# Optimization experiments

Hardware: AMD Instinct MI355X
Metric: run time of the kernel (lower is better)

Reference implementation:

```python
import jax, jax.numpy as jnp
import numpy as np

NSAMPLE = 64  # init kwarg nsample
BN_EPS = 1e-5


def setup_inputs() -> dict:
    key = jax.random.key(0)
    ks = jax.random.split(key, 8)
    B, N = 8, 4096
    C_IN, NC = 6, 3
    NP = 1024
    M = [64, 64, 128]
    C0 = C_IN + NC
    xyz = jax.random.normal(ks[0], (B, 3, N), dtype=jnp.float32)
    points = jax.random.normal(ks[1], (B, C_IN, N), dtype=jnp.float32)
    one_hot_vec = jax.nn.one_hot(jax.random.randint(ks[2], (B,), 0, NC), NC, dtype=jnp.float32)
    idx = jax.random.randint(ks[3], (B, NP), 0, N, dtype=jnp.int64)
    w1 = jax.random.normal(ks[4], (M[0], C0), dtype=jnp.float32) * (1.0 / np.sqrt(C0))
    w2 = jax.random.normal(ks[5], (M[1], M[0]), dtype=jnp.float32) * (1.0 / np.sqrt(M[0]))
    w3 = jax.random.normal(ks[6], (M[2], M[1]), dtype=jnp.float32) * (1.0 / np.sqrt(M[1]))
    g1, b1 = jnp.ones((M[0],), jnp.float32), jnp.zeros((M[0],), jnp.float32)
    g2, b2 = jnp.ones((M[1],), jnp.float32), jnp.zeros((M[1],), jnp.float32)
    g3, b3 = jnp.ones((M[2],), jnp.float32), jnp.zeros((M[2],), jnp.float32)
    return {"xyz": xyz, "points": points, "one_hot_vec": one_hot_vec, "idx": idx,
            "w1": w1, "g1": g1, "b1": b1, "w2": w2, "g2": g2, "b2": b2,
            "w3": w3, "g3": g3, "b3": b3}


def _conv_bn_relu(x, w, gamma, beta):
    # x: (B, C, NP, NS); w: (O, C) -- 1x1 conv, no bias; BN with batch stats (train mode)
    y = jnp.einsum('oc,bcpn->bopn', w, x)
    mu = jnp.mean(y, axis=(0, 2, 3), keepdims=True)
    var = jnp.var(y, axis=(0, 2, 3), keepdims=True)
    y = (y - mu) * jax.lax.rsqrt(var + BN_EPS)
    y = y * gamma[None, :, None, None] + beta[None, :, None, None]
    return jax.nn.relu(y)


def reference(xyz, points, one_hot_vec, idx, w1, g1, b1, w2, g2, b2, w3, g3, b3):
    B, _, N = xyz.shape
    NP = idx.shape[1]
    NS = NSAMPLE
    # concat one-hot class vector onto per-point features: (B, C_in + NC, N)
    feat = jnp.concatenate(
        [points, jnp.broadcast_to(one_hot_vec[:, :, None], (B, one_hot_vec.shape[1], N))], axis=1)
    C = feat.shape[1]
    # gather sampled centers; idx is repeated nsample times in the original,
    # so every sample slot holds the center itself -> broadcast along NS
    gathered = jnp.take_along_axis(feat, idx[:, None, :], axis=2)          # (B, C, NP)
    grouped_points = jnp.broadcast_to(gathered[..., None], (B, C, NP, NS))  # (B, C, NP, NS)
    cx = jnp.take_along_axis(xyz, idx[:, None, :], axis=2)                 # (B, 3, NP)
    cxt = jnp.transpose(cx, (0, 2, 1))[:, :, None, :]                      # (B, NP, 1, 3)
    grouped_xyz = jnp.broadcast_to(cxt - cxt, (B, NP, NS, 3))              # zeros (center-relative)
    # pointwise conv-BN-ReLU MLP, then max over the nsample axis
    x = _conv_bn_relu(grouped_points, w1, g1, b1)
    x = _conv_bn_relu(x, w2, g2, b2)
    x = _conv_bn_relu(x, w3, g3, b3)
    pooled = jnp.max(x, axis=3)  # (B, mlp[-1], NP)
    return grouped_xyz, pooled
```

## Files before the change

### kernel.cpp

```cpp
#include <hip/hip_runtime.h>

constexpr int B    = 8;
constexpr int N    = 4096;
constexpr int CIN  = 6;
constexpr int NC   = 3;
constexpr int NP   = 1024;
constexpr int C0   = CIN + NC;
constexpr int M1   = 64;
constexpr int M2   = 64;
constexpr int M3   = 128;
constexpr int NPTS = B * NP;
constexpr int NPB  = NPTS / 256;
constexpr float EPS = 1e-5f;

constexpr int GZ_ELEMS = B * NP * 64 * 3;
constexpr int GZ_F4    = GZ_ELEMS / 4;
constexpr size_t Y1_OFF = 0;
constexpr size_t Y2_OFF = Y1_OFF + (size_t)M1 * NPTS;
constexpr size_t Y3_OFF = Y2_OFF + (size_t)M2 * NPTS;
constexpr size_t PS1_OFF = Y3_OFF + (size_t)M3 * NPTS;
constexpr size_t PQ1_OFF = PS1_OFF + (size_t)M1 * NPB;
constexpr size_t PS2_OFF = PQ1_OFF + (size_t)M1 * NPB;
constexpr size_t PQ2_OFF = PS2_OFF + (size_t)M2 * NPB;
constexpr size_t PS3_OFF = PQ2_OFF + (size_t)M2 * NPB;
constexpr size_t PQ3_OFF = PS3_OFF + (size_t)M3 * NPB;

template <int OC>
__device__ inline void emit_partials(const float (&acc)[OC], int o0, int pb,
                                     float* __restrict__ ps, float* __restrict__ pq) {
    float sv[OC], qv[OC];
#pragma unroll
    for (int o = 0; o < OC; ++o) { sv[o] = acc[o]; qv[o] = acc[o] * acc[o]; }
#pragma unroll
    for (int off = 32; off; off >>= 1) {
#pragma unroll
        for (int o = 0; o < OC; ++o) {
            sv[o] += __shfl_down(sv[o], off, 64);
            qv[o] += __shfl_down(qv[o], off, 64);
        }
    }
    __shared__ float rs[OC][4], rq[OC][4];
    int lane = threadIdx.x & 63, w = threadIdx.x >> 6;
    if (lane == 0) {
#pragma unroll
        for (int o = 0; o < OC; ++o) { rs[o][w] = sv[o]; rq[o][w] = qv[o]; }
    }
    __syncthreads();
    if (threadIdx.x < OC) {
        int o = threadIdx.x;
        float s = rs[o][0] + rs[o][1] + rs[o][2] + rs[o][3];
        float q = rq[o][0] + rq[o][1] + rq[o][2] + rq[o][3];
        ps[(o0 + o) * NPB + pb] = s;
        pq[(o0 + o) * NPB + pb] = q;
    }
}

template <int CI>
__device__ inline void fold_AB(const float* __restrict__ ps, const float* __restrict__ pq,
                               const float* __restrict__ gamma, const float* __restrict__ beta,
                               float* __restrict__ sAB) {
    int t = threadIdx.x;
    if (t < CI) {
        float s = 0.f, q = 0.f;
#pragma unroll 8
        for (int i = 0; i < NPB; ++i) { s += ps[t * NPB + i]; q += pq[t * NPB + i]; }
        float inv_n = 1.0f / (float)NPTS;
        float mean = s * inv_n;
        float var  = q * inv_n - mean * mean;
        float A = gamma[t] * rsqrtf(var + EPS);
        sAB[2 * t]     = A;
        sAB[2 * t + 1] = beta[t] - mean * A;
    }
}

constexpr int OC1 = 8;
__global__ void k1_gather(const float* __restrict__ points,
                          const float* __restrict__ onehot,
                          const int* __restrict__ idx,
                          const float* __restrict__ w1,
                          float* __restrict__ y1,
                          float* __restrict__ ps1, float* __restrict__ pq1,
                          float4* __restrict__ gz) {
    constexpr int NOB = M1 / OC1;
    __shared__ float ws[OC1 * C0];
    int t = threadIdx.x;
    int ob = blockIdx.x % NOB;
    int pb = blockIdx.x / NOB;
    int o0 = ob * OC1;
    if (t < OC1 * C0) ws[t] = w1[o0 * C0 + t];

    {
        constexpr int PER_BLK = GZ_F4 / (NOB * NPB);
        float4 z = make_float4(0.f, 0.f, 0.f, 0.f);
        float4* g = gz + (size_t)blockIdx.x * PER_BLK + t;
#pragma unroll
        for (int i = 0; i < PER_BLK / 256; ++i) g[i * 256] = z;
    }
    __syncthreads();

    int p  = pb * 256 + t;
    int b  = p >> 10;
    int pp = p & (NP - 1);
    int n  = idx[b * NP + pp];

    float f[C0];
#pragma unroll
    for (int c = 0; c < CIN; ++c) f[c] = points[((size_t)b * CIN + c) * N + n];
#pragma unroll
    for (int c = 0; c < NC; ++c)  f[CIN + c] = onehot[b * NC + c];

    float acc[OC1];
#pragma unroll
    for (int o = 0; o < OC1; ++o) {
        float a = 0.f;
#pragma unroll
        for (int c = 0; c < C0; ++c) a += ws[o * C0 + c] * f[c];
        acc[o] = a;
        y1[(size_t)(o0 + o) * NPTS + p] = a;
    }
    emit_partials<OC1>(acc, o0, pb, ps1, pq1);
}

template <int CI, int CO, int OC>
__global__ void k_mlp(const float* __restrict__ yin,
                      const float* __restrict__ psin, const float* __restrict__ pqin,
                      const float* __restrict__ gamma, const float* __restrict__ beta,
                      const float* __restrict__ w,
                      float* __restrict__ yout,
                      float* __restrict__ psout, float* __restrict__ pqout) {
    constexpr int NOB = CO / OC;
    __shared__ float ws[OC * CI];
    __shared__ float sAB[2 * CI];
    int t = threadIdx.x;
    int ob = blockIdx.x % NOB;
    int pb = blockIdx.x / NOB;
    int o0 = ob * OC;

    fold_AB<CI>(psin, pqin, gamma, beta, sAB);
    for (int i = t; i < OC * CI; i += 256) ws[i] = w[o0 * CI + i];
    __syncthreads();

    int p = pb * 256 + t;
    float x[CI];
#pragma unroll
    for (int c = 0; c < CI; ++c) {
        float v = yin[(size_t)c * NPTS + p] * sAB[2 * c] + sAB[2 * c + 1];
        x[c] = v > 0.f ? v : 0.f;
    }
    float acc[OC];
#pragma unroll
    for (int o = 0; o < OC; ++o) {
        float a = 0.f;
#pragma unroll
        for (int c = 0; c < CI; ++c) a += ws[o * CI + c] * x[c];
        acc[o] = a;
        yout[(size_t)(o0 + o) * NPTS + p] = a;
    }
    __syncthreads();
    emit_partials<OC>(acc, o0, pb, psout, pqout);
}

__global__ void k_out(const float* __restrict__ y3,
                      const float* __restrict__ ps, const float* __restrict__ pq,
                      const float* __restrict__ gamma, const float* __restrict__ beta,
                      float* __restrict__ out) {
    int row = blockIdx.x;
    int c = row & (M3 - 1);
    int b = row >> 7;
    __shared__ float sA, sB;
    int t = threadIdx.x;
    if (t == 0) {
        float s = 0.f, q = 0.f;
#pragma unroll 8
        for (int i = 0; i < NPB; ++i) { s += ps[c * NPB + i]; q += pq[c * NPB + i]; }
        float inv_n = 1.0f / (float)NPTS;
        float mean = s * inv_n;
        float var  = q * inv_n - mean * mean;
        float A = gamma[c] * rsqrtf(var + EPS);
        sA = A;
        sB = beta[c] - mean * A;
    }
    __syncthreads();
    float A = sA, Bb = sB;
    const float4 v = ((const float4*)(y3 + (size_t)c * NPTS + b * NP))[t];
    float4 r;
    r.x = fmaxf(v.x * A + Bb, 0.f);
    r.y = fmaxf(v.y * A + Bb, 0.f);
    r.z = fmaxf(v.z * A + Bb, 0.f);
    r.w = fmaxf(v.w * A + Bb, 0.f);
    ((float4*)(out + (size_t)row * NP))[t] = r;
}

extern "C" void kernel_launch(void* const* d_in, const int* in_sizes, int n_in,
                              void* d_out, int out_size, void* d_ws, size_t ws_size,
                              hipStream_t stream) {
    const float* points = (const float*)d_in[1];
    const float* onehot = (const float*)d_in[2];
    const int*   idx    = (const int*)d_in[3];
    const float* w1 = (const float*)d_in[4];
    const float* g1 = (const float*)d_in[5];
    const float* b1 = (const float*)d_in[6];
    const float* w2 = (const float*)d_in[7];
    const float* g2 = (const float*)d_in[8];
    const float* b2 = (const float*)d_in[9];
    const float* w3 = (const float*)d_in[10];
    const float* g3 = (const float*)d_in[11];
    const float* b3 = (const float*)d_in[12];

    float* out = (float*)d_out;
    float* ws  = (float*)d_ws;
    float* y1  = ws + Y1_OFF;
    float* y2  = ws + Y2_OFF;
    float* y3  = ws + Y3_OFF;
    float* ps1 = ws + PS1_OFF;  float* pq1 = ws + PQ1_OFF;
    float* ps2 = ws + PS2_OFF;  float* pq2 = ws + PQ2_OFF;
    float* ps3 = ws + PS3_OFF;  float* pq3 = ws + PQ3_OFF;

    const int T = 256;

    k1_gather<<<(M1 / OC1) * NPB, T, 0, stream>>>(points, onehot, idx, w1,
                                                  y1, ps1, pq1, (float4*)d_out);
    k_mlp<M1, M2, 8><<<(M2 / 8) * NPB, T, 0, stream>>>(y1, ps1, pq1, g1, b1, w2,
                                                       y2, ps2, pq2);
    k_mlp<M2, M3, 8><<<(M3 / 8) * NPB, T, 0, stream>>>(y2, ps2, pq2, g2, b2, w3,
                                                       y3, ps3, pq3);
    k_out<<<B * M3, T, 0, stream>>>(y3, ps3, pq3, g3, b3, out + GZ_ELEMS);
}
```

Measured before the change: 37.02 us.

## Spread grouped_xyz zero-fill across all four kernels with nontemporal stores

```diff
diff --git a/kernel.cpp b/kernel.cpp
--- a/kernel.cpp
+++ b/kernel.cpp
@@ -13,8 +13,12 @@
 constexpr int NPB  = NPTS / 256;
 constexpr float EPS = 1e-5f;
 
+typedef float f4 __attribute__((ext_vector_type(4)));
+
 constexpr int GZ_ELEMS = B * NP * 64 * 3;
 constexpr int GZ_F4    = GZ_ELEMS / 4;
+constexpr int ZSL      = GZ_F4 / 4;
+
 constexpr size_t Y1_OFF = 0;
 constexpr size_t Y2_OFF = Y1_OFF + (size_t)M1 * NPTS;
 constexpr size_t Y3_OFF = Y2_OFF + (size_t)M2 * NPTS;
@@ -24,6 +28,13 @@
 constexpr size_t PQ2_OFF = PS2_OFF + (size_t)M2 * NPB;
 constexpr size_t PS3_OFF = PQ2_OFF + (size_t)M2 * NPB;
 constexpr size_t PQ3_OFF = PS3_OFF + (size_t)M3 * NPB;
+
+__device__ inline void zero_slice(f4* __restrict__ gz, int sl, int nthreads) {
+    f4 z = {0.f, 0.f, 0.f, 0.f};
+    int gid = blockIdx.x * blockDim.x + threadIdx.x;
+    for (int i = gid; i < ZSL; i += nthreads)
+        __builtin_nontemporal_store(z, &gz[sl * ZSL + i]);
+}
 
 template <int OC>
 __device__ inline void emit_partials(const float (&acc)[OC], int o0, int pb,
@@ -80,22 +91,15 @@
                           const float* __restrict__ w1,
                           float* __restrict__ y1,
                           float* __restrict__ ps1, float* __restrict__ pq1,
-                          float4* __restrict__ gz) {
+                          f4* __restrict__ gz) {
     constexpr int NOB = M1 / OC1;
+    zero_slice(gz, 0, NOB * NPB * 256);
     __shared__ float ws[OC1 * C0];
     int t = threadIdx.x;
     int ob = blockIdx.x % NOB;
     int pb = blockIdx.x / NOB;
     int o0 = ob * OC1;
     if (t < OC1 * C0) ws[t] = w1[o0 * C0 + t];
-
-    {
-        constexpr int PER_BLK = GZ_F4 / (NOB * NPB);
-        float4 z = make_float4(0.f, 0.f, 0.f, 0.f);
-        float4* g = gz + (size_t)blockIdx.x * PER_BLK + t;
-#pragma unroll
-        for (int i = 0; i < PER_BLK / 256; ++i) g[i * 256] = z;
-    }
     __syncthreads();
 
     int p  = pb * 256 + t;
@@ -121,14 +125,16 @@
     emit_partials<OC1>(acc, o0, pb, ps1, pq1);
 }
 
-template <int CI, int CO, int OC>
+template <int CI, int CO, int OC, int SL>
 __global__ void k_mlp(const float* __restrict__ yin,
                       const float* __restrict__ psin, const float* __restrict__ pqin,
                       const float* __restrict__ gamma, const float* __restrict__ beta,
                       const float* __restrict__ w,
                       float* __restrict__ yout,
-                      float* __restrict__ psout, float* __restrict__ pqout) {
+                      float* __restrict__ psout, float* __restrict__ pqout,
+                      f4* __restrict__ gz) {
     constexpr int NOB = CO / OC;
+    zero_slice(gz, SL, NOB * NPB * 256);
     __shared__ float ws[OC * CI];
     __shared__ float sAB[2 * CI];
     int t = threadIdx.x;
@@ -163,7 +169,8 @@
 __global__ void k_out(const float* __restrict__ y3,
                       const float* __restrict__ ps, const float* __restrict__ pq,
                       const float* __restrict__ gamma, const float* __restrict__ beta,
-                      float* __restrict__ out) {
+                      float* __restrict__ out, f4* __restrict__ gz) {
+    zero_slice(gz, 3, B * M3 * 256);
     int row = blockIdx.x;
     int c = row & (M3 - 1);
     int b = row >> 7;
@@ -183,12 +190,12 @@
     __syncthreads();
     float A = sA, Bb = sB;
     const float4 v = ((const float4*)(y3 + (size_t)c * NPTS + b * NP))[t];
-    float4 r;
+    f4 r;
     r.x = fmaxf(v.x * A + Bb, 0.f);
     r.y = fmaxf(v.y * A + Bb, 0.f);
     r.z = fmaxf(v.z * A + Bb, 0.f);
     r.w = fmaxf(v.w * A + Bb, 0.f);
-    ((float4*)(out + (size_t)row * NP))[t] = r;
+    __builtin_nontemporal_store(r, (f4*)(out + (size_t)row * NP) + t);
 }
 
 extern "C" void kernel_launch(void* const* d_in, const int* in_sizes, int n_in,
@@ -215,14 +222,15 @@
     float* ps1 = ws + PS1_OFF;  float* pq1 = ws + PQ1_OFF;
     float* ps2 = ws + PS2_OFF;  float* pq2 = ws + PQ2_OFF;
     float* ps3 = ws + PS3_OFF;  float* pq3 = ws + PQ3_OFF;
+    f4* gz = (f4*)d_out;
 
     const int T = 256;
 
     k1_gather<<<(M1 / OC1) * NPB, T, 0, stream>>>(points, onehot, idx, w1,
-                                                  y1, ps1, pq1, (float4*)d_out);
-    k_mlp<M1, M2, 8><<<(M2 / 8) * NPB, T, 0, stream>>>(y1, ps1, pq1, g1, b1, w2,
-                                                       y2, ps2, pq2);
-    k_mlp<M2, M3, 8><<<(M3 / 8) * NPB, T, 0, stream>>>(y2, ps2, pq2, g2, b2, w3,
-                                                       y3, ps3, pq3);
-    k_out<<<B * M3, T, 0, stream>>>(y3, ps3, pq3, g3, b3, out + GZ_ELEMS);
-}
+                                                  y1, ps1, pq1, gz);
+    k_mlp<M1, M2, 8, 1><<<(M2 / 8) * NPB, T, 0, stream>>>(y1, ps1, pq1, g1, b1, w2,
+                                                          y2, ps2, pq2, gz);
+    k_mlp<M2, M3, 8, 2><<<(M3 / 8) * NPB, T, 0, stream>>>(y2, ps2, pq2, g2, b2, w3,
+                                                          y3, ps3, pq3, gz);
+    k_out<<<B * M3, T, 0, stream>>>(y3, ps3, pq3, g3, b3, out + GZ_ELEMS, gz);
+}
```

New measurement: 37.09 us. No clear change (+0.2%).
